# Optimization experiments

Hardware: AMD Instinct MI355X
Metric: run time of the kernel (lower is better)

Reference implementation:

```python
import jax, jax.numpy as jnp
import numpy as np

N_NODES = 50000


def binarize(w):
    # straight-through sign binarization (forward: sign, backward: identity)
    return w + jax.lax.stop_gradient(jnp.sign(w) - w)


def sage_conv(x, src, dst, w_l, b_l, w_r, num_nodes):
    # PyG SAGEConv with mean aggregation:
    # out[i] = lin_l(mean_{j in N(i)} x[j]) + lin_r(x[i])
    msgs = x[src]  # [E, F] gather from source nodes
    agg = jax.ops.segment_sum(msgs, dst, num_segments=num_nodes)  # [N, F]
    deg = jax.ops.segment_sum(jnp.ones_like(dst, dtype=x.dtype), dst,
                              num_segments=num_nodes)
    agg = agg / jnp.maximum(deg, 1.0)[:, None]
    return agg @ w_l.T + b_l + x @ w_r.T


def setup_inputs() -> dict:
    key = jax.random.key(0)
    ks = jax.random.split(key, 9)
    in_dim, hid, out_dim = 96, 128, 64
    x = jax.random.normal(ks[0], (N_NODES, in_dim), dtype=jnp.float32)
    edge_index = jax.random.randint(ks[1], (2, 800000), 0, N_NODES, dtype=jnp.int64)
    s1 = 1.0 / np.sqrt(in_dim)
    s2 = 1.0 / np.sqrt(hid)
    w1_l = jax.random.uniform(ks[2], (hid, in_dim), minval=-s1, maxval=s1)
    b1 = jax.random.uniform(ks[3], (hid,), minval=-s1, maxval=s1)
    w1_r = jax.random.uniform(ks[4], (hid, in_dim), minval=-s1, maxval=s1)
    w2_l = jax.random.uniform(ks[5], (out_dim, hid), minval=-s2, maxval=s2)
    b2 = jax.random.uniform(ks[6], (out_dim,), minval=-s2, maxval=s2)
    w2_r = jax.random.uniform(ks[7], (out_dim, hid), minval=-s2, maxval=s2)
    return {"x": x, "edge_index": edge_index, "w1_l": w1_l, "b1": b1,
            "w1_r": w1_r, "w2_l": w2_l, "b2": b2, "w2_r": w2_r}


def reference(x, edge_index, w1_l, b1, w1_r, w2_l, b2, w2_r):
    src, dst = edge_index[0], edge_index[1]
    h = sage_conv(x, src, dst, binarize(w1_l), b1, binarize(w1_r), N_NODES)
    h = jax.nn.relu(h)
    out = sage_conv(h, src, dst, binarize(w2_l), b2, binarize(w2_r), N_NODES)
    return jnp.squeeze(out, axis=-1) if out.shape[-1] == 1 else out
```

## Files before the change

kernel.cpp:

```cpp
#include <hip/hip_runtime.h>
#include <cstdint>
#include <cstddef>


#define N_NODES 50000
#define IN_DIM 96
#define HID 128
#define OUT_DIM 64

typedef __attribute__((ext_vector_type(8))) short bf16x8;
typedef __attribute__((ext_vector_type(4))) float f32x4;

static inline size_t alignUp(size_t v, size_t a) { return (v + a - 1) & ~(a - 1); }

__device__ __forceinline__ uint16_t f2bf(float f) {
  uint32_t u = __float_as_uint(f);
  return (uint16_t)((u + 0x7FFF + ((u >> 16) & 1)) >> 16);
}
__device__ __forceinline__ float bflo(uint32_t v) { return __uint_as_float(v << 16); }
__device__ __forceinline__ float bfhi(uint32_t v) { return __uint_as_float(v & 0xFFFF0000u); }

__global__ __launch_bounds__(256) void bucket_count_kernel(const int* __restrict__ dst,
    int* __restrict__ bucketCnt, int E) {
  __shared__ int h[256];
  const int t = threadIdx.x;
  h[t] = 0;
  __syncthreads();
  const int stride = gridDim.x * 256;
  for (int i = blockIdx.x * 256 + t; i < E; i += stride)
    atomicAdd(&h[dst[i] >> 8], 1);
  __syncthreads();
  if (h[t]) atomicAdd(&bucketCnt[t], h[t]);
}

__global__ __launch_bounds__(256) void bucket_scan_kernel(const int* __restrict__ bucketCnt,
    int* __restrict__ bucketBase, int* __restrict__ bucketCursor, int* __restrict__ rowptr,
    int nB, int N) {
  __shared__ int smem[256];
  const int t = threadIdx.x;
  const int v = (t < nB) ? bucketCnt[t] : 0;
  smem[t] = v;
  __syncthreads();
  for (int off = 1; off < 256; off <<= 1) {
    int u = (t >= off) ? smem[t - off] : 0;
    __syncthreads();
    smem[t] += u;
    __syncthreads();
  }
  if (t < nB) {
    const int excl = smem[t] - v;
    bucketBase[t] = excl;
    bucketCursor[t] = excl;
  }
  if (t == 255) {
    bucketBase[nB] = smem[255];
    rowptr[N] = smem[255];
  }
}

#define SCAT_CHUNK 2048
__global__ __launch_bounds__(256) void bucket_scatter_kernel(const int* __restrict__ src,
    const int* __restrict__ dst, int* __restrict__ bucketCursor,
    uint32_t* __restrict__ bucketBuf, int E) {
  __shared__ int h[256];
  __shared__ int g[256];
  __shared__ int c[256];
  const int t = threadIdx.x;
  const int base = blockIdx.x * SCAT_CHUNK;
  const int end = min(base + SCAT_CHUNK, E);
  h[t] = 0;
  __syncthreads();
  for (int i = base + t; i < end; i += 256)
    atomicAdd(&h[dst[i] >> 8], 1);
  __syncthreads();
  if (h[t]) g[t] = atomicAdd(&bucketCursor[t], h[t]);
  c[t] = 0;
  __syncthreads();
  for (int i = base + t; i < end; i += 256) {
    const int d = dst[i];
    const int b = d >> 8;
    const int ticket = atomicAdd(&c[b], 1);
    bucketBuf[g[b] + ticket] = (uint32_t)src[i] | ((uint32_t)(d & 255) << 16);
  }
}

__global__ __launch_bounds__(256) void bucket_build_kernel(const uint32_t* __restrict__ bucketBuf,
    const int* __restrict__ bucketBase, int* __restrict__ rowptr, float* __restrict__ inv_deg,
    uint16_t* __restrict__ adj16, int N) {
  __shared__ int h[256];
  __shared__ int s[256];
  __shared__ int cur[256];
  const int t = threadIdx.x;
  const int b = blockIdx.x;
  const int nodeBase = b << 8;
  const int beg = bucketBase[b], end = bucketBase[b + 1];
  const int m = end - beg;
  h[t] = 0;
  __syncthreads();
  for (int i = t; i < m; i += 256)
    atomicAdd(&h[(bucketBuf[beg + i] >> 16) & 255], 1);
  __syncthreads();
  const int d = h[t];
  s[t] = d;
  __syncthreads();
  for (int off = 1; off < 256; off <<= 1) {
    int u = (t >= off) ? s[t - off] : 0;
    __syncthreads();
    s[t] += u;
    __syncthreads();
  }
  const int excl = s[t] - d;
  const int node = nodeBase + t;
  if (node < N) {
    rowptr[node] = beg + excl;
    inv_deg[node] = 1.0f / (float)(d > 1 ? d : 1);
  }
  cur[t] = excl;
  __syncthreads();
  for (int i = t; i < m; i += 256) {
    const uint32_t u = bucketBuf[beg + i];
    const int ld = (u >> 16) & 255;
    const int ticket = atomicAdd(&cur[ld], 1);
    adj16[beg + ticket] = (uint16_t)(u & 0xFFFFu);
  }
}

__device__ __forceinline__ uint16_t sgnbf(float w) {
  return (w > 0.f) ? (uint16_t)0x3F80 : ((w < 0.f) ? (uint16_t)0xBF80 : (uint16_t)0);
}

#define NS1 (128 * 192)
#define NS2 (128 * 128)
__global__ __launch_bounds__(256) void prep_kernel(const float* __restrict__ x,
    const float* __restrict__ w1l, const float* __restrict__ w1r,
    const float* __restrict__ w2l, const float* __restrict__ w2r,
    uint16_t* __restrict__ S1t, uint16_t* __restrict__ S2t,
    uint16_t* __restrict__ xb, int total4) {
  int idx = blockIdx.x * blockDim.x + threadIdx.x;
  if (idx < NS1) {
    int n = idx / 192, k = idx - n * 192;
    float w = (k < 96) ? w1l[n * 96 + k] : w1r[n * 96 + (k - 96)];
    S1t[idx] = sgnbf(w);
  } else if (idx < NS1 + NS2) {
    int i2 = idx - NS1;
    int n = i2 >> 7, k = i2 & 127;
    float w = (n < 64) ? w2l[n * 128 + k] : w2r[(n - 64) * 128 + k];
    S2t[i2] = sgnbf(w);
  } else {
    int i = idx - NS1 - NS2;
    if (i < total4) {
      float4 v = *(const float4*)(x + (size_t)i * 4);
      uint32_t p0 = (uint32_t)f2bf(v.x) | ((uint32_t)f2bf(v.y) << 16);
      uint32_t p1 = (uint32_t)f2bf(v.z) | ((uint32_t)f2bf(v.w) << 16);
      *(uint2*)(xb + (size_t)i * 4) = make_uint2(p0, p1);
    }
  }
}

__global__ __launch_bounds__(256) void agg1_kernel(const uint16_t* __restrict__ xb,
    const uint16_t* __restrict__ adj16, const int* __restrict__ rowptr,
    const float* __restrict__ inv_deg, uint16_t* __restrict__ AGGb, int nNodes) {
  const int wave = threadIdx.x >> 6;
  const int lane = threadIdx.x & 63;
  const int n = blockIdx.x * 4 + wave;
  if (n >= nNodes) return;
  const int beg = rowptr[n], end = rowptr[n + 1];
  const int g = lane >> 4;
  const int j = lane & 15;
  const bool act = j < 12;
  const int foff = j * 8;
  float a0 = 0.f, a1 = 0.f, a2 = 0.f, a3 = 0.f, a4 = 0.f, a5 = 0.f, a6 = 0.f, a7 = 0.f;

  for (int bb = beg; bb < end; bb += 64) {
    const int cnt = min(64, end - bb);
    const int adjv = (lane < cnt) ? (int)adj16[bb + lane] : 0;
    const int qsteps = (cnt + 3) >> 2;
    int it = 0;
    for (; it + 4 <= qsteps; it += 4) {
      uint4 v[4];
#pragma unroll
      for (int u = 0; u < 4; ++u) {
        const int e = 4 * (it + u) + g;
        const int s = __shfl(adjv, e);
        v[u] = make_uint4(0u, 0u, 0u, 0u);
        if (act && e < cnt) v[u] = *(const uint4*)(xb + (size_t)s * IN_DIM + foff);
      }
      __builtin_amdgcn_sched_barrier(0);
#pragma unroll
      for (int u = 0; u < 4; ++u) {
        a0 += bflo(v[u].x); a1 += bfhi(v[u].x);
        a2 += bflo(v[u].y); a3 += bfhi(v[u].y);
        a4 += bflo(v[u].z); a5 += bfhi(v[u].z);
        a6 += bflo(v[u].w); a7 += bfhi(v[u].w);
      }
    }
    for (; it < qsteps; ++it) {
      const int e = 4 * it + g;
      const int s = __shfl(adjv, e);
      uint4 v = make_uint4(0u, 0u, 0u, 0u);
      if (act && e < cnt) v = *(const uint4*)(xb + (size_t)s * IN_DIM + foff);
      a0 += bflo(v.x); a1 += bfhi(v.x);
      a2 += bflo(v.y); a3 += bfhi(v.y);
      a4 += bflo(v.z); a5 += bfhi(v.z);
      a6 += bflo(v.w); a7 += bfhi(v.w);
    }
  }
  a0 += __shfl_xor(a0, 16); a0 += __shfl_xor(a0, 32);
  a1 += __shfl_xor(a1, 16); a1 += __shfl_xor(a1, 32);
  a2 += __shfl_xor(a2, 16); a2 += __shfl_xor(a2, 32);
  a3 += __shfl_xor(a3, 16); a3 += __shfl_xor(a3, 32);
  a4 += __shfl_xor(a4, 16); a4 += __shfl_xor(a4, 32);
  a5 += __shfl_xor(a5, 16); a5 += __shfl_xor(a5, 32);
  a6 += __shfl_xor(a6, 16); a6 += __shfl_xor(a6, 32);
  a7 += __shfl_xor(a7, 16); a7 += __shfl_xor(a7, 32);
  if (g == 0 && act) {
    const float inv = inv_deg[n];
    uint4 o;
    o.x = (uint32_t)f2bf(a0 * inv) | ((uint32_t)f2bf(a1 * inv) << 16);
    o.y = (uint32_t)f2bf(a2 * inv) | ((uint32_t)f2bf(a3 * inv) << 16);
    o.z = (uint32_t)f2bf(a4 * inv) | ((uint32_t)f2bf(a5 * inv) << 16);
    o.w = (uint32_t)f2bf(a6 * inv) | ((uint32_t)f2bf(a7 * inv) << 16);
    *(uint4*)(AGGb + (size_t)n * IN_DIM + foff) = o;
  }
}

__global__ __launch_bounds__(256) void final_kernel(const uint16_t* __restrict__ T2b,
    const float* __restrict__ R2, const uint16_t* __restrict__ adj16,
    const int* __restrict__ rowptr, const float* __restrict__ inv_deg,
    float* __restrict__ out, int nNodes) {
  const int wave = threadIdx.x >> 6;
  const int lane = threadIdx.x & 63;
  const int n = blockIdx.x * 4 + wave;
  if (n >= nNodes) return;
  const int beg = rowptr[n], end = rowptr[n + 1];
  const int g = lane >> 4;
  const int j = lane & 15;
  const int foff = j * 4;
  float a0 = 0.f, a1 = 0.f, a2 = 0.f, a3 = 0.f;

  for (int bb = beg; bb < end; bb += 64) {
    const int cnt = min(64, end - bb);
    const int adjv = (lane < cnt) ? (int)adj16[bb + lane] : 0;
    const int qsteps = (cnt + 3) >> 2;
    int it = 0;
    for (; it + 4 <= qsteps; it += 4) {
      uint2 v[4];
#pragma unroll
      for (int u = 0; u < 4; ++u) {
        const int e = 4 * (it + u) + g;
        const int s = __shfl(adjv, e);
        v[u] = make_uint2(0u, 0u);
        if (e < cnt) v[u] = *(const uint2*)(T2b + (size_t)s * 64 + foff);
      }
      __builtin_amdgcn_sched_barrier(0);
#pragma unroll
      for (int u = 0; u < 4; ++u) {
        a0 += bflo(v[u].x); a1 += bfhi(v[u].x);
        a2 += bflo(v[u].y); a3 += bfhi(v[u].y);
      }
    }
    for (; it < qsteps; ++it) {
      const int e = 4 * it + g;
      const int s = __shfl(adjv, e);
      uint2 v = make_uint2(0u, 0u);
      if (e < cnt) v = *(const uint2*)(T2b + (size_t)s * 64 + foff);
      a0 += bflo(v.x); a1 += bfhi(v.x);
      a2 += bflo(v.y); a3 += bfhi(v.y);
    }
  }
  a0 += __shfl_xor(a0, 16); a0 += __shfl_xor(a0, 32);
  a1 += __shfl_xor(a1, 16); a1 += __shfl_xor(a1, 32);
  a2 += __shfl_xor(a2, 16); a2 += __shfl_xor(a2, 32);
  a3 += __shfl_xor(a3, 16); a3 += __shfl_xor(a3, 32);
  if (g == 0) {
    const float inv = inv_deg[n];
    const float4 r = *(const float4*)(R2 + (size_t)n * 64 + foff);
    float4 o;
    o.x = a0 * inv + r.x;
    o.y = a1 * inv + r.y;
    o.z = a2 * inv + r.z;
    o.w = a3 * inv + r.w;
    *(float4*)(out + (size_t)n * 64 + foff) = o;
  }
}

#define SP1 200
#define SP2 136
#define HP 136
__global__ __launch_bounds__(256) void gemm12_kernel(
    const uint16_t* __restrict__ AGGb, const uint16_t* __restrict__ xb,
    const uint16_t* __restrict__ S1t, const uint16_t* __restrict__ S2t,
    const float* __restrict__ b1, const float* __restrict__ b2,
    uint16_t* __restrict__ T2b, float* __restrict__ R2, int M) {
  __shared__ uint16_t BS[128 * SP1];
  __shared__ uint16_t Hs[64 * HP];
  const int tid = threadIdx.x;
  const int wv = tid >> 6;
  const int lane = tid & 63;
  const int m16 = lane & 15;
  const int quad = lane >> 4;
  const int rowBase = blockIdx.x * 64 + wv * 16;
  int arow = rowBase + m16;
  if (arow >= M) arow = M - 1;
  const int kq = quad * 8;

#pragma unroll
  for (int i = 0; i < 12; ++i) {
    const int idx8 = tid + i * 256;
    const int col = idx8 / 24;
    const int k8 = (idx8 - col * 24) * 8;
    const bf16x8 v = *(const bf16x8*)(S1t + (size_t)idx8 * 8);
    *(bf16x8*)&BS[col * SP1 + k8] = v;
  }
  bf16x8 a1f[6];
#pragma unroll
  for (int s = 0; s < 3; ++s)
    a1f[s] = *(const bf16x8*)(AGGb + (size_t)arow * IN_DIM + s * 32 + kq);
#pragma unroll
  for (int s = 0; s < 3; ++s)
    a1f[3 + s] = *(const bf16x8*)(xb + (size_t)arow * IN_DIM + s * 32 + kq);
  __syncthreads();

  f32x4 acc1[8];
#pragma unroll
  for (int cf = 0; cf < 8; ++cf) acc1[cf] = (f32x4){0.f, 0.f, 0.f, 0.f};
#pragma unroll
  for (int s = 0; s < 6; ++s) {
#pragma unroll
    for (int cf = 0; cf < 8; ++cf) {
      const bf16x8 b = *(const bf16x8*)&BS[(cf * 16 + m16) * SP1 + s * 32 + kq];
      acc1[cf] = __builtin_amdgcn_mfma_f32_16x16x32_bf16(a1f[s], b, acc1[cf], 0, 0, 0);
    }
  }

#pragma unroll
  for (int cf = 0; cf < 8; ++cf) {
    const int col = cf * 16 + m16;
    const float bias = b1[col];
#pragma unroll
    for (int r = 0; r < 4; ++r) {
      const float v = fmaxf(acc1[cf][r] + bias, 0.f);
      Hs[(wv * 16 + quad * 4 + r) * HP + col] = f2bf(v);
    }
  }
  __syncthreads();

#pragma unroll
  for (int i = 0; i < 8; ++i) {
    const int idx8 = tid + i * 256;
    const int col = idx8 >> 4;
    const int k8 = (idx8 & 15) * 8;
    const bf16x8 v = *(const bf16x8*)(S2t + (size_t)idx8 * 8);
    *(bf16x8*)&BS[col * SP2 + k8] = v;
  }
  __syncthreads();

  f32x4 acc2[8];
#pragma unroll
  for (int cf = 0; cf < 8; ++cf) acc2[cf] = (f32x4){0.f, 0.f, 0.f, 0.f};
#pragma unroll
  for (int s = 0; s < 4; ++s) {
    const bf16x8 a = *(const bf16x8*)&Hs[(wv * 16 + m16) * HP + s * 32 + kq];
#pragma unroll
    for (int cf = 0; cf < 8; ++cf) {
      const bf16x8 b = *(const bf16x8*)&BS[(cf * 16 + m16) * SP2 + s * 32 + kq];
      acc2[cf] = __builtin_amdgcn_mfma_f32_16x16x32_bf16(a, b, acc2[cf], 0, 0, 0);
    }
  }

#pragma unroll
  for (int cf = 0; cf < 8; ++cf) {
    const int col = cf * 16 + m16;
#pragma unroll
    for (int r = 0; r < 4; ++r) {
      const int row = rowBase + quad * 4 + r;
      if (row < M) {
        const float v = acc2[cf][r];
        if (col < 64) {
          T2b[(size_t)row * 64 + col] = f2bf(v);
        } else {
          R2[(size_t)row * 64 + (col - 64)] = v + b2[col - 64];
        }
      }
    }
  }
}

extern "C" void kernel_launch(void* const* d_in, const int* in_sizes, int n_in,
                              void* d_out, int out_size, void* d_ws, size_t ws_size,
                              hipStream_t stream) {
  const float* x   = (const float*)d_in[0];
  const int*   ei  = (const int*)d_in[1];
  const float* w1l = (const float*)d_in[2];
  const float* b1  = (const float*)d_in[3];
  const float* w1r = (const float*)d_in[4];
  const float* w2l = (const float*)d_in[5];
  const float* b2  = (const float*)d_in[6];
  const float* w2r = (const float*)d_in[7];
  float* out = (float*)d_out;

  const int N = in_sizes[0] / IN_DIM;
  const int E = in_sizes[1] / 2;
  const int* src = ei;
  const int* dst = ei + E;
  const int NB = (N + 255) >> 8;

  char* p = (char*)d_ws;
  uint16_t* AGGb = (uint16_t*)p; p += alignUp((size_t)N * IN_DIM * sizeof(uint16_t), 256);
  uint16_t* T2b  = (uint16_t*)p; p += alignUp((size_t)N * 64 * sizeof(uint16_t), 256);
  float* R2      = (float*)p;    p += alignUp((size_t)N * 64 * sizeof(float), 256);
  uint16_t* xb = (uint16_t*)p; p += alignUp((size_t)N * IN_DIM * sizeof(uint16_t), 256);
  uint16_t* S1t = (uint16_t*)p; p += alignUp(NS1 * sizeof(uint16_t), 256);
  uint16_t* S2t = (uint16_t*)p; p += alignUp(NS2 * sizeof(uint16_t), 256);
  int* rowptr = (int*)p; p += alignUp((size_t)(N + 1) * sizeof(int), 256);
  float* inv_deg = (float*)p; p += alignUp((size_t)N * sizeof(float), 256);
  uint16_t* adj16 = (uint16_t*)p; p += alignUp((size_t)E * sizeof(uint16_t), 256);
  uint32_t* bucketBuf = (uint32_t*)p; p += alignUp((size_t)E * sizeof(uint32_t), 256);
  int* bucketCnt = (int*)p;    p += alignUp(256 * sizeof(int), 256);
  int* bucketBase = (int*)p;   p += alignUp(257 * sizeof(int), 256);
  int* bucketCursor = (int*)p; p += alignUp(256 * sizeof(int), 256);
  (void)ws_size; (void)n_in; (void)out_size;

  hipMemsetAsync(bucketCnt, 0, 256 * sizeof(int), stream);

  bucket_count_kernel<<<256, 256, 0, stream>>>(dst, bucketCnt, E);
  bucket_scan_kernel<<<1, 256, 0, stream>>>(bucketCnt, bucketBase, bucketCursor, rowptr, NB, N);
  bucket_scatter_kernel<<<(E + SCAT_CHUNK - 1) / SCAT_CHUNK, 256, 0, stream>>>(
      src, dst, bucketCursor, bucketBuf, E);
  bucket_build_kernel<<<NB, 256, 0, stream>>>(bucketBuf, bucketBase, rowptr, inv_deg, adj16, N);

  const int total4 = N * IN_DIM / 4;
  const int prepThreads = NS1 + NS2 + total4;
  prep_kernel<<<(prepThreads + 255) / 256, 256, 0, stream>>>(x, w1l, w1r, w2l, w2r,
                                                             S1t, S2t, xb, total4);

  const int nodeBlocks = (N + 3) / 4;
  agg1_kernel<<<nodeBlocks, 256, 0, stream>>>(xb, adj16, rowptr, inv_deg, AGGb, N);

  const int gemmBlocks = (N + 63) / 64;
  gemm12_kernel<<<gemmBlocks, 256, 0, stream>>>(AGGb, xb, S1t, S2t, b1, b2, T2b, R2, N);

  final_kernel<<<nodeBlocks, 256, 0, stream>>>(T2b, R2, adj16, rowptr, inv_deg, out, N);
}
```

Before: 188.2 us.

## Map one node per 16-lane group in aggregation and drop global atomics

```diff
diff --git a/kernel.cpp b/kernel.cpp
--- a/kernel.cpp
+++ b/kernel.cpp
@@ -21,7 +21,7 @@
 __device__ __forceinline__ float bfhi(uint32_t v) { return __uint_as_float(v & 0xFFFF0000u); }
 
 __global__ __launch_bounds__(256) void bucket_count_kernel(const int* __restrict__ dst,
-    int* __restrict__ bucketCnt, int E) {
+    int* __restrict__ bucketPart, int E) {
   __shared__ int h[256];
   const int t = threadIdx.x;
   h[t] = 0;
@@ -30,15 +30,17 @@
   for (int i = blockIdx.x * 256 + t; i < E; i += stride)
     atomicAdd(&h[dst[i] >> 8], 1);
   __syncthreads();
-  if (h[t]) atomicAdd(&bucketCnt[t], h[t]);
-}
-
-__global__ __launch_bounds__(256) void bucket_scan_kernel(const int* __restrict__ bucketCnt,
+  bucketPart[blockIdx.x * 256 + t] = h[t];
+}
+
+__global__ __launch_bounds__(256) void bucket_scan_kernel(const int* __restrict__ bucketPart,
     int* __restrict__ bucketBase, int* __restrict__ bucketCursor, int* __restrict__ rowptr,
     int nB, int N) {
   __shared__ int smem[256];
   const int t = threadIdx.x;
-  const int v = (t < nB) ? bucketCnt[t] : 0;
+  int v = 0;
+  for (int b = 0; b < 256; ++b) v += bucketPart[b * 256 + t];
+  if (t >= nB) v = 0;
   smem[t] = v;
   __syncthreads();
   for (int off = 1; off < 256; off <<= 1) {
@@ -85,7 +87,7 @@
 }
 
 __global__ __launch_bounds__(256) void bucket_build_kernel(const uint32_t* __restrict__ bucketBuf,
-    const int* __restrict__ bucketBase, int* __restrict__ rowptr, float* __restrict__ inv_deg,
+    const int* __restrict__ bucketBase, int* __restrict__ rowptr,
     uint16_t* __restrict__ adj16, int N) {
   __shared__ int h[256];
   __shared__ int s[256];
@@ -111,10 +113,7 @@
   }
   const int excl = s[t] - d;
   const int node = nodeBase + t;
-  if (node < N) {
-    rowptr[node] = beg + excl;
-    inv_deg[node] = 1.0f / (float)(d > 1 ? d : 1);
-  }
+  if (node < N) rowptr[node] = beg + excl;
   cur[t] = excl;
   __syncthreads();
   for (int i = t; i < m; i += 256) {
@@ -159,62 +158,48 @@
 
 __global__ __launch_bounds__(256) void agg1_kernel(const uint16_t* __restrict__ xb,
     const uint16_t* __restrict__ adj16, const int* __restrict__ rowptr,
-    const float* __restrict__ inv_deg, uint16_t* __restrict__ AGGb, int nNodes) {
-  const int wave = threadIdx.x >> 6;
-  const int lane = threadIdx.x & 63;
-  const int n = blockIdx.x * 4 + wave;
+    uint16_t* __restrict__ AGGb, int nNodes) {
+  const int sg = threadIdx.x >> 4;
+  const int j = threadIdx.x & 15;
+  const int n = blockIdx.x * 16 + sg;
   if (n >= nNodes) return;
   const int beg = rowptr[n], end = rowptr[n + 1];
-  const int g = lane >> 4;
-  const int j = lane & 15;
   const bool act = j < 12;
   const int foff = j * 8;
   float a0 = 0.f, a1 = 0.f, a2 = 0.f, a3 = 0.f, a4 = 0.f, a5 = 0.f, a6 = 0.f, a7 = 0.f;
 
-  for (int bb = beg; bb < end; bb += 64) {
-    const int cnt = min(64, end - bb);
-    const int adjv = (lane < cnt) ? (int)adj16[bb + lane] : 0;
-    const int qsteps = (cnt + 3) >> 2;
-    int it = 0;
-    for (; it + 4 <= qsteps; it += 4) {
-      uint4 v[4];
-#pragma unroll
-      for (int u = 0; u < 4; ++u) {
-        const int e = 4 * (it + u) + g;
-        const int s = __shfl(adjv, e);
-        v[u] = make_uint4(0u, 0u, 0u, 0u);
-        if (act && e < cnt) v[u] = *(const uint4*)(xb + (size_t)s * IN_DIM + foff);
-      }
-      __builtin_amdgcn_sched_barrier(0);
-#pragma unroll
-      for (int u = 0; u < 4; ++u) {
-        a0 += bflo(v[u].x); a1 += bfhi(v[u].x);
-        a2 += bflo(v[u].y); a3 += bfhi(v[u].y);
-        a4 += bflo(v[u].z); a5 += bfhi(v[u].z);
-        a6 += bflo(v[u].w); a7 += bfhi(v[u].w);
-      }
-    }
-    for (; it < qsteps; ++it) {
-      const int e = 4 * it + g;
-      const int s = __shfl(adjv, e);
-      uint4 v = make_uint4(0u, 0u, 0u, 0u);
-      if (act && e < cnt) v = *(const uint4*)(xb + (size_t)s * IN_DIM + foff);
-      a0 += bflo(v.x); a1 += bfhi(v.x);
-      a2 += bflo(v.y); a3 += bfhi(v.y);
-      a4 += bflo(v.z); a5 += bfhi(v.z);
-      a6 += bflo(v.w); a7 += bfhi(v.w);
-    }
-  }
-  a0 += __shfl_xor(a0, 16); a0 += __shfl_xor(a0, 32);
-  a1 += __shfl_xor(a1, 16); a1 += __shfl_xor(a1, 32);
-  a2 += __shfl_xor(a2, 16); a2 += __shfl_xor(a2, 32);
-  a3 += __shfl_xor(a3, 16); a3 += __shfl_xor(a3, 32);
-  a4 += __shfl_xor(a4, 16); a4 += __shfl_xor(a4, 32);
-  a5 += __shfl_xor(a5, 16); a5 += __shfl_xor(a5, 32);
-  a6 += __shfl_xor(a6, 16); a6 += __shfl_xor(a6, 32);
-  a7 += __shfl_xor(a7, 16); a7 += __shfl_xor(a7, 32);
-  if (g == 0 && act) {
-    const float inv = inv_deg[n];
+  int e = beg;
+  for (; e + 4 <= end; e += 4) {
+    const int s0 = adj16[e], s1 = adj16[e + 1], s2 = adj16[e + 2], s3 = adj16[e + 3];
+    uint4 v0 = make_uint4(0u,0u,0u,0u), v1 = v0, v2 = v0, v3 = v0;
+    if (act) {
+      v0 = *(const uint4*)(xb + (size_t)s0 * IN_DIM + foff);
+      v1 = *(const uint4*)(xb + (size_t)s1 * IN_DIM + foff);
+      v2 = *(const uint4*)(xb + (size_t)s2 * IN_DIM + foff);
+      v3 = *(const uint4*)(xb + (size_t)s3 * IN_DIM + foff);
+    }
+    __builtin_amdgcn_sched_barrier(0);
+    a0 += bflo(v0.x) + bflo(v1.x) + bflo(v2.x) + bflo(v3.x);
+    a1 += bfhi(v0.x) + bfhi(v1.x) + bfhi(v2.x) + bfhi(v3.x);
+    a2 += bflo(v0.y) + bflo(v1.y) + bflo(v2.y) + bflo(v3.y);
+    a3 += bfhi(v0.y) + bfhi(v1.y) + bfhi(v2.y) + bfhi(v3.y);
+    a4 += bflo(v0.z) + bflo(v1.z) + bflo(v2.z) + bflo(v3.z);
+    a5 += bfhi(v0.z) + bfhi(v1.z) + bfhi(v2.z) + bfhi(v3.z);
+    a6 += bflo(v0.w) + bflo(v1.w) + bflo(v2.w) + bflo(v3.w);
+    a7 += bfhi(v0.w) + bfhi(v1.w) + bfhi(v2.w) + bfhi(v3.w);
+  }
+  for (; e < end; ++e) {
+    const int s = adj16[e];
+    uint4 v = make_uint4(0u,0u,0u,0u);
+    if (act) v = *(const uint4*)(xb + (size_t)s * IN_DIM + foff);
+    a0 += bflo(v.x); a1 += bfhi(v.x);
+    a2 += bflo(v.y); a3 += bfhi(v.y);
+    a4 += bflo(v.z); a5 += bfhi(v.z);
+    a6 += bflo(v.w); a7 += bfhi(v.w);
+  }
+  if (act) {
+    const int d = end - beg;
+    const float inv = 1.0f / (float)(d > 1 ? d : 1);
     uint4 o;
     o.x = (uint32_t)f2bf(a0 * inv) | ((uint32_t)f2bf(a1 * inv) << 16);
     o.y = (uint32_t)f2bf(a2 * inv) | ((uint32_t)f2bf(a3 * inv) << 16);
@@ -226,62 +211,43 @@
 
 __global__ __launch_bounds__(256) void final_kernel(const uint16_t* __restrict__ T2b,
     const float* __restrict__ R2, const uint16_t* __restrict__ adj16,
-    const int* __restrict__ rowptr, const float* __restrict__ inv_deg,
-    float* __restrict__ out, int nNodes) {
-  const int wave = threadIdx.x >> 6;
-  const int lane = threadIdx.x & 63;
-  const int n = blockIdx.x * 4 + wave;
+    const int* __restrict__ rowptr, float* __restrict__ out, int nNodes) {
+  const int sg = threadIdx.x >> 4;
+  const int j = threadIdx.x & 15;
+  const int n = blockIdx.x * 16 + sg;
   if (n >= nNodes) return;
   const int beg = rowptr[n], end = rowptr[n + 1];
-  const int g = lane >> 4;
-  const int j = lane & 15;
   const int foff = j * 4;
   float a0 = 0.f, a1 = 0.f, a2 = 0.f, a3 = 0.f;
 
-  for (int bb = beg; bb < end; bb += 64) {
-    const int cnt = min(64, end - bb);
-    const int adjv = (lane < cnt) ? (int)adj16[bb + lane] : 0;
-    const int qsteps = (cnt + 3) >> 2;
-    int it = 0;
-    for (; it + 4 <= qsteps; it += 4) {
-      uint2 v[4];
-#pragma unroll
-      for (int u = 0; u < 4; ++u) {
-        const int e = 4 * (it + u) + g;
-        const int s = __shfl(adjv, e);
-        v[u] = make_uint2(0u, 0u);
-        if (e < cnt) v[u] = *(const uint2*)(T2b + (size_t)s * 64 + foff);
-      }
-      __builtin_amdgcn_sched_barrier(0);
-#pragma unroll
-      for (int u = 0; u < 4; ++u) {
-        a0 += bflo(v[u].x); a1 += bfhi(v[u].x);
-        a2 += bflo(v[u].y); a3 += bfhi(v[u].y);
-      }
-    }
-    for (; it < qsteps; ++it) {
-      const int e = 4 * it + g;
-      const int s = __shfl(adjv, e);
-      uint2 v = make_uint2(0u, 0u);
-      if (e < cnt) v = *(const uint2*)(T2b + (size_t)s * 64 + foff);
-      a0 += bflo(v.x); a1 += bfhi(v.x);
-      a2 += bflo(v.y); a3 += bfhi(v.y);
-    }
-  }
-  a0 += __shfl_xor(a0, 16); a0 += __shfl_xor(a0, 32);
-  a1 += __shfl_xor(a1, 16); a1 += __shfl_xor(a1, 32);
-  a2 += __shfl_xor(a2, 16); a2 += __shfl_xor(a2, 32);
-  a3 += __shfl_xor(a3, 16); a3 += __shfl_xor(a3, 32);
-  if (g == 0) {
-    const float inv = inv_deg[n];
-    const float4 r = *(const float4*)(R2 + (size_t)n * 64 + foff);
-    float4 o;
-    o.x = a0 * inv + r.x;
-    o.y = a1 * inv + r.y;
-    o.z = a2 * inv + r.z;
-    o.w = a3 * inv + r.w;
-    *(float4*)(out + (size_t)n * 64 + foff) = o;
-  }
+  int e = beg;
+  for (; e + 4 <= end; e += 4) {
+    const int s0 = adj16[e], s1 = adj16[e + 1], s2 = adj16[e + 2], s3 = adj16[e + 3];
+    const uint2 v0 = *(const uint2*)(T2b + (size_t)s0 * 64 + foff);
+    const uint2 v1 = *(const uint2*)(T2b + (size_t)s1 * 64 + foff);
+    const uint2 v2 = *(const uint2*)(T2b + (size_t)s2 * 64 + foff);
+    const uint2 v3 = *(const uint2*)(T2b + (size_t)s3 * 64 + foff);
+    __builtin_amdgcn_sched_barrier(0);
+    a0 += bflo(v0.x) + bflo(v1.x) + bflo(v2.x) + bflo(v3.x);
+    a1 += bfhi(v0.x) + bfhi(v1.x) + bfhi(v2.x) + bfhi(v3.x);
+    a2 += bflo(v0.y) + bflo(v1.y) + bflo(v2.y) + bflo(v3.y);
+    a3 += bfhi(v0.y) + bfhi(v1.y) + bfhi(v2.y) + bfhi(v3.y);
+  }
+  for (; e < end; ++e) {
+    const int s = adj16[e];
+    const uint2 v = *(const uint2*)(T2b + (size_t)s * 64 + foff);
+    a0 += bflo(v.x); a1 += bfhi(v.x);
+    a2 += bflo(v.y); a3 += bfhi(v.y);
+  }
+  const int d = end - beg;
+  const float inv = 1.0f / (float)(d > 1 ? d : 1);
+  const float4 r = *(const float4*)(R2 + (size_t)n * 64 + foff);
+  float4 o;
+  o.x = a0 * inv + r.x;
+  o.y = a1 * inv + r.y;
+  o.z = a2 * inv + r.z;
+  o.w = a3 * inv + r.w;
+  *(float4*)(out + (size_t)n * 64 + foff) = o;
 }
 
 #define SP1 200
@@ -413,32 +379,29 @@
   uint16_t* S1t = (uint16_t*)p; p += alignUp(NS1 * sizeof(uint16_t), 256);
   uint16_t* S2t = (uint16_t*)p; p += alignUp(NS2 * sizeof(uint16_t), 256);
   int* rowptr = (int*)p; p += alignUp((size_t)(N + 1) * sizeof(int), 256);
-  float* inv_deg = (float*)p; p += alignUp((size_t)N * sizeof(float), 256);
   uint16_t* adj16 = (uint16_t*)p; p += alignUp((size_t)E * sizeof(uint16_t), 256);
   uint32_t* bucketBuf = (uint32_t*)p; p += alignUp((size_t)E * sizeof(uint32_t), 256);
-  int* bucketCnt = (int*)p;    p += alignUp(256 * sizeof(int), 256);
+  int* bucketPart = (int*)p;   p += alignUp(256 * 256 * sizeof(int), 256);
   int* bucketBase = (int*)p;   p += alignUp(257 * sizeof(int), 256);
   int* bucketCursor = (int*)p; p += alignUp(256 * sizeof(int), 256);
   (void)ws_size; (void)n_in; (void)out_size;
 
-  hipMemsetAsync(bucketCnt, 0, 256 * sizeof(int), stream);
-
-  bucket_count_kernel<<<256, 256, 0, stream>>>(dst, bucketCnt, E);
-  bucket_scan_kernel<<<1, 256, 0, stream>>>(bucketCnt, bucketBase, bucketCursor, rowptr, NB, N);
+  bucket_count_kernel<<<256, 256, 0, stream>>>(dst, bucketPart, E);
+  bucket_scan_kernel<<<1, 256, 0, stream>>>(bucketPart, bucketBase, bucketCursor, rowptr, NB, N);
   bucket_scatter_kernel<<<(E + SCAT_CHUNK - 1) / SCAT_CHUNK, 256, 0, stream>>>(
       src, dst, bucketCursor, bucketBuf, E);
-  bucket_build_kernel<<<NB, 256, 0, stream>>>(bucketBuf, bucketBase, rowptr, inv_deg, adj16, N);
+  bucket_build_kernel<<<NB, 256, 0, stream>>>(bucketBuf, bucketBase, rowptr, adj16, N);
 
   const int total4 = N * IN_DIM / 4;
   const int prepThreads = NS1 + NS2 + total4;
   prep_kernel<<<(prepThreads + 255) / 256, 256, 0, stream>>>(x, w1l, w1r, w2l, w2r,
                                                              S1t, S2t, xb, total4);
 
-  const int nodeBlocks = (N + 3) / 4;
-  agg1_kernel<<<nodeBlocks, 256, 0, stream>>>(xb, adj16, rowptr, inv_deg, AGGb, N);
+  const int nodeBlocks16 = (N + 15) / 16;
+  agg1_kernel<<<nodeBlocks16, 256, 0, stream>>>(xb, adj16, rowptr, AGGb, N);
 
   const int gemmBlocks = (N + 63) / 64;
   gemm12_kernel<<<gemmBlocks, 256, 0, stream>>>(AGGb, xb, S1t, S2t, b1, b2, T2b, R2, N);
 
-  final_kernel<<<nodeBlocks, 256, 0, stream>>>(T2b, R2, adj16, rowptr, inv_deg, out, N);
-}
+  final_kernel<<<nodeBlocks16, 256, 0, stream>>>(T2b, R2, adj16, rowptr, out, N);
+}
```

Measured after the change: 187.9 us. About the same (-0.1%).
